# Kernel tuning notes

Measured on AMD Instinct MI355X. Metric: run time of the kernel, lower is better.

## Reference

```python
import jax, jax.numpy as jnp
import numpy as np

BS, P, D = 64, 300, 1024
NUM_CLASSES = 150


def setup_inputs() -> dict:
    key = jax.random.key(0)
    ks = jax.random.split(key, 12)
    s = 0.02
    return {
        "x": jax.random.normal(ks[0], (BS * P, D), jnp.float32),
        "subject": jax.random.normal(ks[1], (BS, D), jnp.float32),
        "obj": jax.random.normal(ks[2], (BS, D), jnp.float32),
        "relation": jax.random.normal(ks[3], (BS, D), jnp.float32),
        "W_theta": jax.random.normal(ks[4], (D, D), jnp.float32) * s,
        "b_theta": jax.random.normal(ks[5], (D,), jnp.float32) * s,
        "W_pair": jax.random.normal(ks[6], (3 * D, 1), jnp.float32) * s,
        "b_pair": jax.random.normal(ks[7], (1,), jnp.float32) * s,
        "W_cls": jax.random.normal(ks[8], (2 * D, 1), jnp.float32) * s,
        "b_cls": jax.random.normal(ks[9], (1,), jnp.float32) * s,
        "W_bbox": jax.random.normal(ks[10], (D, (NUM_CLASSES + 1) * 4), jnp.float32) * s,
        "b_bbox": jax.random.normal(ks[11], ((NUM_CLASSES + 1) * 4,), jnp.float32) * s,
    }


def reference(x, subject, obj, relation, W_theta, b_theta, W_pair, b_pair,
              W_cls, b_cls, W_bbox, b_bbox):
    bs = relation.shape[0]
    rel = relation @ W_theta + b_theta  # (bs, D)
    xb = x.reshape(bs, P, D)

    # cls_score_pair(concat([x1, x2, rel])) decomposed into 3 sliced matmuls.
    # x1[b,i,j] = x[b,j] (cols), x2[b,i,j] = x[b,i] (rows).
    Wa, Wb, Wc = W_pair[:D, 0], W_pair[D:2 * D, 0], W_pair[2 * D:, 0]
    col_term = xb @ Wa          # (bs, P) -> broadcast over rows i
    row_term = xb @ Wb          # (bs, P) -> broadcast over cols j
    rel_term = rel @ Wc + b_pair[0]  # (bs,)
    pair_score = jax.nn.sigmoid(row_term[:, :, None] + col_term[None if False else slice(None), None, :]
                                + rel_term[:, None, None])  # (bs, P, P)

    # cls_score on [x, subject] and [x, object]
    W1, W2 = W_cls[:D, 0], W_cls[D:, 0]
    xw = xb @ W1                                  # (bs, P)
    s_score = jax.nn.sigmoid(xw + (subject @ W2 + b_cls[0])[:, None])  # (bs, P)
    o_score = jax.nn.sigmoid(xw + (obj @ W2 + b_cls[0])[:, None])      # (bs, P)

    pair_score = pair_score * o_score[:, None, :] * s_score[:, :, None]

    x_subj = jnp.stack([1.0 - s_score, s_score], axis=-1).reshape(-1, 2)
    x_obj = jnp.stack([1.0 - o_score, o_score], axis=-1).reshape(-1, 2)

    bbox_deltas = x @ W_bbox + b_bbox  # (bs*P, (C+1)*4)
    return (x_subj, x_obj, pair_score, bbox_deltas)
```

## Files before the change

kernel.cpp:

```cpp
#include <hip/hip_runtime.h>

#define PP    300
#define DD    1024
#define NOUT  604
#define NROWS 19200
#define OFF_PAIR  76800
#define OFF_BBOX  5836800

typedef unsigned short u16;
typedef __attribute__((ext_vector_type(8))) short bf16x8;
typedef __attribute__((ext_vector_type(4))) float f32x4;

#define GLOBAL_AS __attribute__((address_space(1)))
#define LDS_AS    __attribute__((address_space(3)))

__device__ inline u16 f2bf(float f) {
    unsigned u = __float_as_uint(f);
    return (u16)((u + 0x7fffu + ((u >> 16) & 1u)) >> 16);
}
__device__ inline float dot4(float4 a, float4 b) {
    return fmaf(a.x, b.x, fmaf(a.y, b.y, fmaf(a.z, b.z, a.w * b.w)));
}
__device__ inline float sigmoidf(float z) { return 1.f / (1.f + __expf(-z)); }

__global__ void k_transpose(const float* __restrict__ W, u16* __restrict__ Bt) {
    __shared__ float tile[32][33];
    int k0 = blockIdx.x * 32;
    int n0 = blockIdx.y * 32;
    int tx = threadIdx.x;
    int ty = threadIdx.y;
#pragma unroll
    for (int i = 0; i < 4; ++i) {
        int k = k0 + ty + i * 8;
        int n = n0 + tx;
        tile[ty + i * 8][tx] = (n < NOUT) ? W[(size_t)k * NOUT + n] : 0.f;
    }
    __syncthreads();
#pragma unroll
    for (int i = 0; i < 4; ++i) {
        int n = n0 + ty + i * 8;
        int k = k0 + tx;
        Bt[(size_t)n * DD + k] = f2bf(tile[tx][ty + i * 8]);
    }
}

__global__ void k_vtheta(const float* __restrict__ Wt, const float* __restrict__ Wpair,
                         float* __restrict__ v) {
    int wave = threadIdx.x >> 6, lane = threadIdx.x & 63;
    int k = blockIdx.x * 4 + wave;
    const float4* row = (const float4*)(Wt + (size_t)k * DD);
    const float4* wc  = (const float4*)(Wpair + 2 * DD);
    float s = 0.f;
#pragma unroll
    for (int i = 0; i < 4; ++i) s += dot4(row[i * 64 + lane], wc[i * 64 + lane]);
#pragma unroll
    for (int off = 32; off; off >>= 1) s += __shfl_down(s, off, 64);
    if (lane == 0) v[k] = s;
}

__global__ void k_scalars(const float* __restrict__ relation, const float* __restrict__ subject,
                          const float* __restrict__ obj, const float* __restrict__ btheta,
                          const float* __restrict__ Wpair, const float* __restrict__ bpair,
                          const float* __restrict__ Wcls, const float* __restrict__ bcls,
                          const float* __restrict__ v,
                          float* __restrict__ relt, float* __restrict__ subc,
                          float* __restrict__ objc) {
    __shared__ float red[4];
    int wave = threadIdx.x >> 6, lane = threadIdx.x & 63;
    int b = blockIdx.x;
    const float4* aa;
    const float4* bb;
    if (wave == 0)      { aa = (const float4*)(relation + (size_t)b * DD); bb = (const float4*)v; }
    else if (wave == 1) { aa = (const float4*)(subject + (size_t)b * DD);  bb = (const float4*)(Wcls + DD); }
    else if (wave == 2) { aa = (const float4*)(obj + (size_t)b * DD);      bb = (const float4*)(Wcls + DD); }
    else                { aa = (const float4*)btheta;                      bb = (const float4*)(Wpair + 2 * DD); }
    float s = 0.f;
#pragma unroll
    for (int i = 0; i < 4; ++i) s += dot4(aa[i * 64 + lane], bb[i * 64 + lane]);
#pragma unroll
    for (int off = 32; off; off >>= 1) s += __shfl_down(s, off, 64);
    if (lane == 0) red[wave] = s;
    __syncthreads();
    if (threadIdx.x == 0) {
        relt[b] = red[0] + red[3] + bpair[0];
        subc[b] = red[1] + bcls[0];
        objc[b] = red[2] + bcls[0];
    }
}

template<int WB>
__global__ __launch_bounds__(256) void k_rows(
        const float* __restrict__ x, const float* __restrict__ Wpair,
        const float* __restrict__ Wcls,
        const float* __restrict__ relt, const float* __restrict__ subc,
        const float* __restrict__ objc,
        float* __restrict__ colv, float* __restrict__ rowp,
        float* __restrict__ sarr, float* __restrict__ oarr,
        float* __restrict__ out, u16* __restrict__ xb) {
    int wave = threadIdx.x >> 6, lane = threadIdx.x & 63;
    int r = blockIdx.x * 4 + wave;
    const float4* xr = (const float4*)(x + (size_t)r * DD);
    const float4* wa = (const float4*)(Wpair);
    const float4* wb = (const float4*)(Wpair + DD);
    const float4* w1 = (const float4*)(Wcls);
    float ca = 0.f, cb = 0.f, cw = 0.f;
#pragma unroll
    for (int i = 0; i < 4; ++i) {
        int idx = i * 64 + lane;
        float4 xv = xr[idx];
        ca += dot4(xv, wa[idx]);
        cb += dot4(xv, wb[idx]);
        cw += dot4(xv, w1[idx]);
        if (WB) {
            unsigned lo = __builtin_amdgcn_perm(__float_as_uint(xv.y), __float_as_uint(xv.x), 0x07060302u);
            unsigned hi = __builtin_amdgcn_perm(__float_as_uint(xv.w), __float_as_uint(xv.z), 0x07060302u);
            *(uint2*)(xb + (size_t)r * DD + idx * 4) = make_uint2(lo, hi);
        }
    }
#pragma unroll
    for (int off = 32; off; off >>= 1) {
        ca += __shfl_down(ca, off, 64);
        cb += __shfl_down(cb, off, 64);
        cw += __shfl_down(cw, off, 64);
    }
    if (lane == 0) {
        int b = r / 300;
        float s = sigmoidf(cw + subc[b]);
        float o = sigmoidf(cw + objc[b]);
        colv[r] = ca;
        rowp[r] = cb + relt[b];
        sarr[r] = s;
        oarr[r] = o;
        ((float2*)out)[r]         = make_float2(1.f - s, s);
        ((float2*)out)[NROWS + r] = make_float2(1.f - o, o);
    }
}

#define PR_ROWS 10
__global__ __launch_bounds__(192) void k_pair(
        const float* __restrict__ rowp, const float* __restrict__ colv,
        const float* __restrict__ sarr, const float* __restrict__ oarr,
        float* __restrict__ pout) {
    __shared__ float cb_s[300];
    __shared__ float ob_s[300];
    int blk = blockIdx.x;
    int b = blk / 30;
    int chunk = blk - b * 30;
    int r0 = b * 300 + chunk * PR_ROWS;
    int tid = threadIdx.x;
    for (int j = tid; j < 300; j += 192) {
        cb_s[j] = colv[b * 300 + j];
        ob_s[j] = oarr[b * 300 + j];
    }
    __syncthreads();
    if (tid < 150) {
        float c0 = cb_s[2 * tid],     c1 = cb_s[2 * tid + 1];
        float o0 = ob_s[2 * tid],     o1 = ob_s[2 * tid + 1];
#pragma unroll
        for (int rr = 0; rr < PR_ROWS; ++rr) {
            int r = r0 + rr;
            float rp = rowp[r];
            float ss = sarr[r];
            float p0 = sigmoidf(rp + c0) * o0 * ss;
            float p1 = sigmoidf(rp + c1) * o1 * ss;
            ((float2*)(pout + (size_t)r * 300))[tid] = make_float2(p0, p1);
        }
    }
}

#define BKK 64
__global__ __launch_bounds__(256) void k_gemm_bf(
        const u16* __restrict__ xb, const u16* __restrict__ bt,
        const float* __restrict__ bias, float* __restrict__ out) {
    __shared__ u16 As[128 * BKK] __attribute__((aligned(16)));
    __shared__ u16 Bs[128 * BKK] __attribute__((aligned(16)));

    int bid = blockIdx.x;
    int xcd = bid & 7;
    int rest = bid >> 3;
    int n_t = rest % 5;
    int m_t = (rest / 5) * 8 + xcd;
    if (m_t >= 150) return;

    int tid = threadIdx.x;
    int wave = tid >> 6;
    int lane = tid & 63;
    int wr = wave >> 1, wc = wave & 1;
    int quad = lane >> 4;
    int l16 = lane & 15;

    f32x4 acc[4][4] = {};

    const u16* a_base = xb + (size_t)m_t * 128 * DD;
    const u16* b_base = bt + (size_t)n_t * 128 * DD;
    int s_row = lane >> 3;
    int s_c16 = (lane & 7) ^ s_row;

    for (int k0 = 0; k0 < DD; k0 += BKK) {
#pragma unroll
        for (int q = 0; q < 4; ++q) {
            int rowblk = q * 32 + wave * 8;
            const u16* ga = a_base + (size_t)(rowblk + s_row) * DD + k0 + s_c16 * 8;
            __builtin_amdgcn_global_load_lds((const GLOBAL_AS unsigned int*)ga,
                                             (LDS_AS unsigned int*)(As + rowblk * BKK),
                                             16, 0, 0);
            const u16* gb = b_base + (size_t)(rowblk + s_row) * DD + k0 + s_c16 * 8;
            __builtin_amdgcn_global_load_lds((const GLOBAL_AS unsigned int*)gb,
                                             (LDS_AS unsigned int*)(Bs + rowblk * BKK),
                                             16, 0, 0);
        }
        __syncthreads();
#pragma unroll
        for (int kk = 0; kk < BKK; kk += 32) {
            bf16x8 af[4], bfv[4];
            int cx = (((kk >> 3) + quad) ^ (l16 & 7)) * 8;
#pragma unroll
            for (int f = 0; f < 4; ++f) {
                int m = wr * 64 + f * 16 + l16;
                af[f] = *(const bf16x8*)(As + m * BKK + cx);
                int n = wc * 64 + f * 16 + l16;
                bfv[f] = *(const bf16x8*)(Bs + n * BKK + cx);
            }
#pragma unroll
            for (int fi = 0; fi < 4; ++fi)
#pragma unroll
                for (int fj = 0; fj < 4; ++fj)
                    acc[fi][fj] = __builtin_amdgcn_mfma_f32_16x16x32_bf16(
                        af[fi], bfv[fj], acc[fi][fj], 0, 0, 0);
        }
        __syncthreads();
    }

#pragma unroll
    for (int fj = 0; fj < 4; ++fj) {
        int col = n_t * 128 + wc * 64 + fj * 16 + l16;
        if (col < NOUT) {
            float bia = bias[col];
#pragma unroll
            for (int fi = 0; fi < 4; ++fi) {
#pragma unroll
                for (int rg = 0; rg < 4; ++rg) {
                    int row = m_t * 128 + wr * 64 + fi * 16 + quad * 4 + rg;
                    out[(size_t)row * NOUT + col] = acc[fi][fj][rg] + bia;
                }
            }
        }
    }
}

__global__ __launch_bounds__(256) void k_gemm(
        const float* __restrict__ x, const u16* __restrict__ bt,
        const float* __restrict__ bias, float* __restrict__ out) {
    __shared__ u16 As[128 * BKK] __attribute__((aligned(16)));
    __shared__ u16 Bs[128 * BKK] __attribute__((aligned(16)));

    int bid = blockIdx.x;
    int xcd = bid & 7;
    int rest = bid >> 3;
    int n_t = rest % 5;
    int m_t = (rest / 5) * 8 + xcd;
    if (m_t >= 150) return;

    int tid = threadIdx.x;
    int wave = tid >> 6;
    int lane = tid & 63;
    int wr = wave >> 1, wc = wave & 1;
    int quad = lane >> 4;
    int l16 = lane & 15;

    f32x4 acc[4][4] = {};

    const float* a_base = x  + (size_t)m_t * 128 * DD;
    const u16*   b_base = bt + (size_t)n_t * 128 * DD;
    int s_row = lane >> 3;
    int s_c16 = lane & 7;
    int arow8 = tid >> 4;
    int acol4 = tid & 15;

    for (int k0 = 0; k0 < DD; k0 += BKK) {
#pragma unroll
        for (int q = 0; q < 4; ++q) {
            int rowblk = q * 32 + wave * 8;
            const u16* gb = b_base + (size_t)(rowblk + s_row) * DD + k0 + s_c16 * 8;
            __builtin_amdgcn_global_load_lds((const GLOBAL_AS unsigned int*)gb,
                                             (LDS_AS unsigned int*)(Bs + rowblk * BKK),
                                             16, 0, 0);
        }
#pragma unroll
        for (int it = 0; it < 8; ++it) {
            int row = it * 16 + arow8;
            float4 av = *(const float4*)(a_base + (size_t)row * DD + k0 + acol4 * 4);
            unsigned lo = __builtin_amdgcn_perm(__float_as_uint(av.y), __float_as_uint(av.x), 0x07060302u);
            unsigned hi = __builtin_amdgcn_perm(__float_as_uint(av.w), __float_as_uint(av.z), 0x07060302u);
            *(uint2*)(As + row * BKK + acol4 * 4) = make_uint2(lo, hi);
        }
        __syncthreads();
#pragma unroll
        for (int kk = 0; kk < BKK; kk += 32) {
            bf16x8 af[4], bfv[4];
#pragma unroll
            for (int f = 0; f < 4; ++f) {
                int m = wr * 64 + f * 16 + l16;
                af[f] = *(const bf16x8*)(As + m * BKK + kk + quad * 8);
                int n = wc * 64 + f * 16 + l16;
                bfv[f] = *(const bf16x8*)(Bs + n * BKK + kk + quad * 8);
            }
#pragma unroll
            for (int fi = 0; fi < 4; ++fi)
#pragma unroll
                for (int fj = 0; fj < 4; ++fj)
                    acc[fi][fj] = __builtin_amdgcn_mfma_f32_16x16x32_bf16(
                        af[fi], bfv[fj], acc[fi][fj], 0, 0, 0);
        }
        __syncthreads();
    }

#pragma unroll
    for (int fj = 0; fj < 4; ++fj) {
        int col = n_t * 128 + wc * 64 + fj * 16 + l16;
        if (col < NOUT) {
            float bia = bias[col];
#pragma unroll
            for (int fi = 0; fi < 4; ++fi) {
#pragma unroll
                for (int rg = 0; rg < 4; ++rg) {
                    int row = m_t * 128 + wr * 64 + fi * 16 + quad * 4 + rg;
                    out[(size_t)row * NOUT + col] = acc[fi][fj][rg] + bia;
                }
            }
        }
    }
}

extern "C" void kernel_launch(void* const* d_in, const int* in_sizes, int n_in,
                              void* d_out, int out_size, void* d_ws, size_t ws_size,
                              hipStream_t stream) {
    const void* P[12] = {};
    int sv[3] = {-1, -1, -1}; int nsv = 0;
    int sc[2] = {-1, -1};     int nsc = 0;
    for (int i = 0; i < n_in; ++i) {
        switch (in_sizes[i]) {
            case 19660800: P[0]  = d_in[i]; break;
            case 65536:    if (nsv < 3) sv[nsv++] = i; break;
            case 1048576:  P[4]  = d_in[i]; break;
            case 1024:     P[5]  = d_in[i]; break;
            case 3072:     P[6]  = d_in[i]; break;
            case 1:        if (nsc < 2) sc[nsc++] = i; break;
            case 2048:     P[8]  = d_in[i]; break;
            case 618496:   P[10] = d_in[i]; break;
            case 604:      P[11] = d_in[i]; break;
            default: break;
        }
    }
    bool alpha = (n_in == 12 && in_sizes[0] == 618496);
    if (alpha) {
        P[2] = d_in[sv[0]]; P[3] = d_in[sv[1]]; P[1] = d_in[sv[2]];
        P[9] = d_in[sc[0]]; P[7] = d_in[sc[1]];
    } else {
        P[1] = d_in[sv[0]]; P[2] = d_in[sv[1]]; P[3] = d_in[sv[2]];
        P[7] = d_in[sc[0]]; P[9] = d_in[sc[1]];
    }
    const float* x        = (const float*)P[0];
    const float* subject  = (const float*)P[1];
    const float* obj      = (const float*)P[2];
    const float* relation = (const float*)P[3];
    const float* W_theta  = (const float*)P[4];
    const float* b_theta  = (const float*)P[5];
    const float* W_pair   = (const float*)P[6];
    const float* b_pair   = (const float*)P[7];
    const float* W_cls    = (const float*)P[8];
    const float* b_cls    = (const float*)P[9];
    const float* W_bbox   = (const float*)P[10];
    const float* b_bbox   = (const float*)P[11];
    float* out = (float*)d_out;

    char* ws = (char*)d_ws;
    float* v    = (float*)(ws + 0);
    float* relt = (float*)(ws + 4096);
    float* subc = (float*)(ws + 4352);
    float* objc = (float*)(ws + 4608);
    float* colv = (float*)(ws + 4864);
    float* rowp = (float*)(ws + 81664);
    float* sarr = (float*)(ws + 158464);
    float* oarr = (float*)(ws + 235264);
    u16*   Bt   = (u16*)(ws + 312064);
    u16*   Xb   = (u16*)(ws + 1622784);

    const size_t WS_NEED_BF16 = 40944384;
    bool big_ws = (ws_size >= WS_NEED_BF16);

    k_transpose<<<dim3(32, 20), dim3(32, 8), 0, stream>>>(W_bbox, Bt);
    k_vtheta<<<256, 256, 0, stream>>>(W_theta, W_pair, v);
    k_scalars<<<64, 256, 0, stream>>>(relation, subject, obj, b_theta, W_pair, b_pair,
                                      W_cls, b_cls, v, relt, subc, objc);
    if (big_ws) {
        k_rows<1><<<4800, 256, 0, stream>>>(x, W_pair, W_cls, relt, subc, objc,
                                            colv, rowp, sarr, oarr, out, Xb);
    } else {
        k_rows<0><<<4800, 256, 0, stream>>>(x, W_pair, W_cls, relt, subc, objc,
                                            colv, rowp, sarr, oarr, out, nullptr);
    }
    k_pair<<<1920, 192, 0, stream>>>(rowp, colv, sarr, oarr, out + OFF_PAIR);
    if (big_ws) {
        k_gemm_bf<<<760, 256, 0, stream>>>(Xb, Bt, b_bbox, out + OFF_BBOX);
    } else {
        k_gemm<<<760, 256, 0, stream>>>(x, Bt, b_bbox, out + OFF_BBOX);
    }
}
```

Baseline: 224.7 us.

## Fuse pair-score and bbox GEMM into one launch with double-buffered LDS

Merges the W_bbox transpose and the theta-vector reduction into one prep kernel. Runs the pair-score blocks and the bf16 bbox GEMM blocks inside a single kernel, so the memory-bound pair writes can overlap with the MFMA GEMM work. The GEMM K loop now double-buffers its LDS tiles, issuing the next global_load_lds before computing on the current tile. This cuts two launches and should hide load latency, at the cost of double the LDS per block, which may lower occupancy.

```diff
diff --git a/kernel.cpp b/kernel.cpp
--- a/kernel.cpp
+++ b/kernel.cpp
@@ -23,39 +23,42 @@
 }
 __device__ inline float sigmoidf(float z) { return 1.f / (1.f + __expf(-z)); }
 
-__global__ void k_transpose(const float* __restrict__ W, u16* __restrict__ Bt) {
+__global__ __launch_bounds__(256) void k_prep(const float* __restrict__ Wbbox, u16* __restrict__ Bt,
+                                              const float* __restrict__ Wt, const float* __restrict__ Wpair,
+                                              float* __restrict__ v) {
     __shared__ float tile[32][33];
-    int k0 = blockIdx.x * 32;
-    int n0 = blockIdx.y * 32;
-    int tx = threadIdx.x;
-    int ty = threadIdx.y;
-#pragma unroll
-    for (int i = 0; i < 4; ++i) {
-        int k = k0 + ty + i * 8;
-        int n = n0 + tx;
-        tile[ty + i * 8][tx] = (n < NOUT) ? W[(size_t)k * NOUT + n] : 0.f;
-    }
-    __syncthreads();
-#pragma unroll
-    for (int i = 0; i < 4; ++i) {
-        int n = n0 + ty + i * 8;
-        int k = k0 + tx;
-        Bt[(size_t)n * DD + k] = f2bf(tile[tx][ty + i * 8]);
-    }
-}
-
-__global__ void k_vtheta(const float* __restrict__ Wt, const float* __restrict__ Wpair,
-                         float* __restrict__ v) {
-    int wave = threadIdx.x >> 6, lane = threadIdx.x & 63;
-    int k = blockIdx.x * 4 + wave;
-    const float4* row = (const float4*)(Wt + (size_t)k * DD);
-    const float4* wc  = (const float4*)(Wpair + 2 * DD);
-    float s = 0.f;
-#pragma unroll
-    for (int i = 0; i < 4; ++i) s += dot4(row[i * 64 + lane], wc[i * 64 + lane]);
-#pragma unroll
-    for (int off = 32; off; off >>= 1) s += __shfl_down(s, off, 64);
-    if (lane == 0) v[k] = s;
+    int blk = blockIdx.x;
+    int tid = threadIdx.x;
+    if (blk < 640) {
+        int k0 = (blk & 31) * 32;
+        int n0 = (blk >> 5) * 32;
+        int tx = tid & 31;
+        int ty = tid >> 5;
+#pragma unroll
+        for (int i = 0; i < 4; ++i) {
+            int k = k0 + ty + i * 8;
+            int n = n0 + tx;
+            tile[ty + i * 8][tx] = (n < NOUT) ? Wbbox[(size_t)k * NOUT + n] : 0.f;
+        }
+        __syncthreads();
+#pragma unroll
+        for (int i = 0; i < 4; ++i) {
+            int n = n0 + ty + i * 8;
+            int k = k0 + tx;
+            Bt[(size_t)n * DD + k] = f2bf(tile[tx][ty + i * 8]);
+        }
+    } else {
+        int wave = tid >> 6, lane = tid & 63;
+        int k = (blk - 640) * 4 + wave;
+        const float4* row = (const float4*)(Wt + (size_t)k * DD);
+        const float4* wc  = (const float4*)(Wpair + 2 * DD);
+        float s = 0.f;
+#pragma unroll
+        for (int i = 0; i < 4; ++i) s += dot4(row[i * 64 + lane], wc[i * 64 + lane]);
+#pragma unroll
+        for (int off = 32; off; off >>= 1) s += __shfl_down(s, off, 64);
+        if (lane == 0) v[k] = s;
+    }
 }
 
 __global__ void k_scalars(const float* __restrict__ relation, const float* __restrict__ subject,
@@ -136,8 +139,132 @@
     }
 }
 
-#define PR_ROWS 10
-__global__ __launch_bounds__(192) void k_pair(
+#define BKK 64
+#define NSTEP 16
+
+#define STAGE_TILE(buf, k0)                                                                  \
+    _Pragma("unroll")                                                                        \
+    for (int q = 0; q < 4; ++q) {                                                            \
+        int rowblk = q * 32 + wave * 8;                                                      \
+        const u16* ga = a_base + (size_t)(rowblk + s_row) * DD + (k0) + s_c16 * 8;           \
+        __builtin_amdgcn_global_load_lds((const GLOBAL_AS unsigned int*)ga,                  \
+                                         (LDS_AS unsigned int*)(As[buf] + rowblk * BKK),     \
+                                         16, 0, 0);                                          \
+        const u16* gb = b_base + (size_t)(rowblk + s_row) * DD + (k0) + s_c16 * 8;           \
+        __builtin_amdgcn_global_load_lds((const GLOBAL_AS unsigned int*)gb,                  \
+                                         (LDS_AS unsigned int*)(Bs[buf] + rowblk * BKK),     \
+                                         16, 0, 0);                                          \
+    }
+
+#define COMPUTE_TILE(buf)                                                                    \
+    _Pragma("unroll")                                                                        \
+    for (int kk = 0; kk < BKK; kk += 32) {                                                   \
+        bf16x8 af[4], bfv[4];                                                                \
+        int cx = (((kk >> 3) + quad) ^ (l16 & 7)) * 8;                                       \
+        _Pragma("unroll")                                                                    \
+        for (int f = 0; f < 4; ++f) {                                                        \
+            int m = wr * 64 + f * 16 + l16;                                                  \
+            af[f] = *(const bf16x8*)(As[buf] + m * BKK + cx);                                \
+            int n = wc * 64 + f * 16 + l16;                                                  \
+            bfv[f] = *(const bf16x8*)(Bs[buf] + n * BKK + cx);                               \
+        }                                                                                    \
+        _Pragma("unroll")                                                                    \
+        for (int fi = 0; fi < 4; ++fi)                                                       \
+            _Pragma("unroll")                                                                \
+            for (int fj = 0; fj < 4; ++fj)                                                   \
+                acc[fi][fj] = __builtin_amdgcn_mfma_f32_16x16x32_bf16(                       \
+                    af[fi], bfv[fj], acc[fi][fj], 0, 0, 0);                                  \
+    }
+
+__global__ __launch_bounds__(256) void k_fused(
+        const u16* __restrict__ xb, const u16* __restrict__ bt,
+        const float* __restrict__ bias, float* __restrict__ outb,
+        const float* __restrict__ rowp, const float* __restrict__ colv,
+        const float* __restrict__ sarr, const float* __restrict__ oarr,
+        float* __restrict__ pout) {
+    __shared__ u16 As[2][128 * BKK] __attribute__((aligned(16)));
+    __shared__ u16 Bs[2][128 * BKK] __attribute__((aligned(16)));
+
+    int gbid = blockIdx.x;
+    if (gbid < 760) {
+        int xcd = gbid & 7;
+        int rest = gbid >> 3;
+        int n_t = rest % 5;
+        int m_t = (rest / 5) * 8 + xcd;
+        if (m_t >= 150) return;
+
+        int tid = threadIdx.x;
+        int wave = tid >> 6;
+        int lane = tid & 63;
+        int wr = wave >> 1, wc = wave & 1;
+        int quad = lane >> 4;
+        int l16 = lane & 15;
+
+        f32x4 acc[4][4] = {};
+
+        const u16* a_base = xb + (size_t)m_t * 128 * DD;
+        const u16* b_base = bt + (size_t)n_t * 128 * DD;
+        int s_row = lane >> 3;
+        int s_c16 = (lane & 7) ^ s_row;
+
+        STAGE_TILE(0, 0)
+        __syncthreads();
+
+#pragma unroll 1
+        for (int t = 0; t < NSTEP; t += 2) {
+            STAGE_TILE(1, (t + 1) * BKK)
+            COMPUTE_TILE(0)
+            __syncthreads();
+            if (t + 2 < NSTEP) { STAGE_TILE(0, (t + 2) * BKK) }
+            COMPUTE_TILE(1)
+            __syncthreads();
+        }
+
+#pragma unroll
+        for (int fj = 0; fj < 4; ++fj) {
+            int col = n_t * 128 + wc * 64 + fj * 16 + l16;
+            if (col < NOUT) {
+                float bia = bias[col];
+#pragma unroll
+                for (int fi = 0; fi < 4; ++fi) {
+#pragma unroll
+                    for (int rg = 0; rg < 4; ++rg) {
+                        int row = m_t * 128 + wr * 64 + fi * 16 + quad * 4 + rg;
+                        outb[(size_t)row * NOUT + col] = acc[fi][fj][rg] + bia;
+                    }
+                }
+            }
+        }
+    } else {
+        float* cb_s = (float*)As;
+        float* ob_s = ((float*)As) + 300;
+        int blk = gbid - 760;
+        int b = blk / 30;
+        int chunk = blk - b * 30;
+        int r0 = b * 300 + chunk * 10;
+        int tid = threadIdx.x;
+        for (int j = tid; j < 300; j += 256) {
+            cb_s[j] = colv[b * 300 + j];
+            ob_s[j] = oarr[b * 300 + j];
+        }
+        __syncthreads();
+        if (tid < 150) {
+            float c0 = cb_s[2 * tid], c1 = cb_s[2 * tid + 1];
+            float o0 = ob_s[2 * tid], o1 = ob_s[2 * tid + 1];
+#pragma unroll
+            for (int rr = 0; rr < 10; ++rr) {
+                int r = r0 + rr;
+                float rp = rowp[r];
+                float ss = sarr[r];
+                float p0 = sigmoidf(rp + c0) * o0 * ss;
+                float p1 = sigmoidf(rp + c1) * o1 * ss;
+                ((float2*)(pout + (size_t)r * 300))[tid] = make_float2(p0, p1);
+            }
+        }
+    }
+}
+
+__global__ __launch_bounds__(192) void k_pair_sa(
         const float* __restrict__ rowp, const float* __restrict__ colv,
         const float* __restrict__ sarr, const float* __restrict__ oarr,
         float* __restrict__ pout) {
@@ -146,7 +273,7 @@
     int blk = blockIdx.x;
     int b = blk / 30;
     int chunk = blk - b * 30;
-    int r0 = b * 300 + chunk * PR_ROWS;
+    int r0 = b * 300 + chunk * 10;
     int tid = threadIdx.x;
     for (int j = tid; j < 300; j += 192) {
         cb_s[j] = colv[b * 300 + j];
@@ -154,96 +281,16 @@
     }
     __syncthreads();
     if (tid < 150) {
-        float c0 = cb_s[2 * tid],     c1 = cb_s[2 * tid + 1];
-        float o0 = ob_s[2 * tid],     o1 = ob_s[2 * tid + 1];
-#pragma unroll
-        for (int rr = 0; rr < PR_ROWS; ++rr) {
+        float c0 = cb_s[2 * tid], c1 = cb_s[2 * tid + 1];
+        float o0 = ob_s[2 * tid], o1 = ob_s[2 * tid + 1];
+#pragma unroll
+        for (int rr = 0; rr < 10; ++rr) {
             int r = r0 + rr;
             float rp = rowp[r];
             float ss = sarr[r];
             float p0 = sigmoidf(rp + c0) * o0 * ss;
             float p1 = sigmoidf(rp + c1) * o1 * ss;
             ((float2*)(pout + (size_t)r * 300))[tid] = make_float2(p0, p1);
-        }
-    }
-}
-
-#define BKK 64
-__global__ __launch_bounds__(256) void k_gemm_bf(
-        const u16* __restrict__ xb, const u16* __restrict__ bt,
-        const float* __restrict__ bias, float* __restrict__ out) {
-    __shared__ u16 As[128 * BKK] __attribute__((aligned(16)));
-    __shared__ u16 Bs[128 * BKK] __attribute__((aligned(16)));
-
-    int bid = blockIdx.x;
-    int xcd = bid & 7;
-    int rest = bid >> 3;
-    int n_t = rest % 5;
-    int m_t = (rest / 5) * 8 + xcd;
-    if (m_t >= 150) return;
-
-    int tid = threadIdx.x;
-    int wave = tid >> 6;
-    int lane = tid & 63;
-    int wr = wave >> 1, wc = wave & 1;
-    int quad = lane >> 4;
-    int l16 = lane & 15;
-
-    f32x4 acc[4][4] = {};
-
-    const u16* a_base = xb + (size_t)m_t * 128 * DD;
-    const u16* b_base = bt + (size_t)n_t * 128 * DD;
-    int s_row = lane >> 3;
-    int s_c16 = (lane & 7) ^ s_row;
-
-    for (int k0 = 0; k0 < DD; k0 += BKK) {
-#pragma unroll
-        for (int q = 0; q < 4; ++q) {
-            int rowblk = q * 32 + wave * 8;
-            const u16* ga = a_base + (size_t)(rowblk + s_row) * DD + k0 + s_c16 * 8;
-            __builtin_amdgcn_global_load_lds((const GLOBAL_AS unsigned int*)ga,
-                                             (LDS_AS unsigned int*)(As + rowblk * BKK),
-                                             16, 0, 0);
-            const u16* gb = b_base + (size_t)(rowblk + s_row) * DD + k0 + s_c16 * 8;
-            __builtin_amdgcn_global_load_lds((const GLOBAL_AS unsigned int*)gb,
-                                             (LDS_AS unsigned int*)(Bs + rowblk * BKK),
-                                             16, 0, 0);
-        }
-        __syncthreads();
-#pragma unroll
-        for (int kk = 0; kk < BKK; kk += 32) {
-            bf16x8 af[4], bfv[4];
-            int cx = (((kk >> 3) + quad) ^ (l16 & 7)) * 8;
-#pragma unroll
-            for (int f = 0; f < 4; ++f) {
-                int m = wr * 64 + f * 16 + l16;
-                af[f] = *(const bf16x8*)(As + m * BKK + cx);
-                int n = wc * 64 + f * 16 + l16;
-                bfv[f] = *(const bf16x8*)(Bs + n * BKK + cx);
-            }
-#pragma unroll
-            for (int fi = 0; fi < 4; ++fi)
-#pragma unroll
-                for (int fj = 0; fj < 4; ++fj)
-                    acc[fi][fj] = __builtin_amdgcn_mfma_f32_16x16x32_bf16(
-                        af[fi], bfv[fj], acc[fi][fj], 0, 0, 0);
-        }
-        __syncthreads();
-    }
-
-#pragma unroll
-    for (int fj = 0; fj < 4; ++fj) {
-        int col = n_t * 128 + wc * 64 + fj * 16 + l16;
-        if (col < NOUT) {
-            float bia = bias[col];
-#pragma unroll
-            for (int fi = 0; fi < 4; ++fi) {
-#pragma unroll
-                for (int rg = 0; rg < 4; ++rg) {
-                    int row = m_t * 128 + wr * 64 + fi * 16 + quad * 4 + rg;
-                    out[(size_t)row * NOUT + col] = acc[fi][fj][rg] + bia;
-                }
-            }
         }
     }
 }
@@ -389,21 +436,18 @@
     const size_t WS_NEED_BF16 = 40944384;
     bool big_ws = (ws_size >= WS_NEED_BF16);
 
-    k_transpose<<<dim3(32, 20), dim3(32, 8), 0, stream>>>(W_bbox, Bt);
-    k_vtheta<<<256, 256, 0, stream>>>(W_theta, W_pair, v);
+    k_prep<<<896, 256, 0, stream>>>(W_bbox, Bt, W_theta, W_pair, v);
     k_scalars<<<64, 256, 0, stream>>>(relation, subject, obj, b_theta, W_pair, b_pair,
                                       W_cls, b_cls, v, relt, subc, objc);
     if (big_ws) {
         k_rows<1><<<4800, 256, 0, stream>>>(x, W_pair, W_cls, relt, subc, objc,
                                             colv, rowp, sarr, oarr, out, Xb);
+        k_fused<<<2680, 256, 0, stream>>>(Xb, Bt, b_bbox, out + OFF_BBOX,
+                                          rowp, colv, sarr, oarr, out + OFF_PAIR);
     } else {
         k_rows<0><<<4800, 256, 0, stream>>>(x, W_pair, W_cls, relt, subc, objc,
                                             colv, rowp, sarr, oarr, out, nullptr);
-    }
-    k_pair<<<1920, 192, 0, stream>>>(rowp, colv, sarr, oarr, out + OFF_PAIR);
-    if (big_ws) {
-        k_gemm_bf<<<760, 256, 0, stream>>>(Xb, Bt, b_bbox, out + OFF_BBOX);
-    } else {
+        k_pair_sa<<<1920, 192, 0, stream>>>(rowp, colv, sarr, oarr, out + OFF_PAIR);
         k_gemm<<<760, 256, 0, stream>>>(x, Bt, b_bbox, out + OFF_BBOX);
     }
 }
```

Result: faster. 209.4 us (-6.8%).
